# Kernel tuning notes

Hardware: AMD Instinct MI355X
Metric: run time of the kernel (lower is better)

The kernel has to match this reference:

```python
import jax, jax.numpy as jnp
import numpy as np

HQ, HKV, HD = 8, 4, 256          # query heads, kv heads, head dim
SW = 1024                         # sliding window (layer_idx=0 is even -> window active)
EPS = 1e-6
SCALE = 256.0 ** -0.5             # query_pre_attn_scalar ** -0.5
THETA = 10000.0
NEG = jnp.finfo(jnp.float32).min


def _rms_norm(x, w):
    # Gemma2 RMSNorm: fp32 variance, weight applied as (1 + kernel)
    var = jnp.mean(jnp.square(x.astype(jnp.float32)), axis=-1, keepdims=True)
    xn = x / jnp.sqrt(var + EPS)
    return (1.0 + w) * xn


def _rope(q, k, positions):
    # standard rotate-half RoPE over full head_dim
    inv = 1.0 / (THETA ** (jnp.arange(0, HD, 2, dtype=jnp.float32) / HD))  # [HD/2]
    freqs = positions.astype(jnp.float32)[..., None] * inv                  # [B,S,HD/2]
    emb = jnp.concatenate([freqs, freqs], axis=-1)                          # [B,S,HD]
    cos = jnp.cos(emb)[:, :, None, :]
    sin = jnp.sin(emb)[:, :, None, :]
    def rot(x):
        return jnp.concatenate([-x[..., HD // 2:], x[..., :HD // 2]], axis=-1)
    return q * cos + rot(q) * sin, k * cos + rot(k) * sin


def setup_inputs() -> dict:
    key = jax.random.key(0)
    ks = jax.random.split(key, 12)
    B, S, D, I = 1, 2048, 2304, 9216
    std = 0.02
    return {
        "hidden_states": jax.random.normal(ks[0], (B, S, D), jnp.float32),
        "attention_mask": jnp.ones((B, S), jnp.int32),
        "position_ids": jnp.broadcast_to(jnp.arange(S, dtype=jnp.int32)[None], (B, S)),
        "wq": jax.random.normal(ks[1], (D, HQ * HD), jnp.float32) * std,
        "wk": jax.random.normal(ks[2], (D, HKV * HD), jnp.float32) * std,
        "wv": jax.random.normal(ks[3], (D, HKV * HD), jnp.float32) * std,
        "wo": jax.random.normal(ks[4], (HQ * HD, D), jnp.float32) * std,
        "w_gate": jax.random.normal(ks[5], (D, I), jnp.float32) * std,
        "w_up": jax.random.normal(ks[6], (D, I), jnp.float32) * std,
        "w_down": jax.random.normal(ks[7], (I, D), jnp.float32) * std,
        "ln_in": jax.random.uniform(ks[8], (D,), jnp.float32) * 0.1,
        "ln_post_attn": jax.random.uniform(ks[9], (D,), jnp.float32) * 0.1,
        "ln_pre_ffn": jax.random.uniform(ks[10], (D,), jnp.float32) * 0.1,
        "ln_post_ffn": jax.random.uniform(ks[11], (D,), jnp.float32) * 0.1,
    }


def _attention(h, attention_mask, position_ids, wq, wk, wv, wo):
    B, S, _ = h.shape
    q = (h @ wq).reshape(B, S, HQ, HD)
    k = (h @ wk).reshape(B, S, HKV, HD)
    v = (h @ wv).reshape(B, S, HKV, HD)
    q, k = _rope(q, k, position_ids)
    # GQA: repeat kv heads
    groups = HQ // HKV
    k = jnp.repeat(k, groups, axis=2)  # [B,S,HQ,HD]
    v = jnp.repeat(v, groups, axis=2)
    # combined mask: causal AND within sliding window AND padding mask
    i = jnp.arange(S)[:, None]
    j = jnp.arange(S)[None, :]
    keep = (j <= i) & ((i - j) < SW)                       # [S,S]
    keep = keep[None, None] & (attention_mask[:, None, None, :] > 0)  # [B,1,S,S]
    bias = jnp.where(keep, 0.0, NEG).astype(jnp.float32)
    scores = jnp.einsum("bqhd,bkhd->bhqk", q, k) * SCALE + bias
    probs = jax.nn.softmax(scores, axis=-1)
    out = jnp.einsum("bhqk,bkhd->bqhd", probs, v).reshape(B, S, HQ * HD)
    return out @ wo


def reference(hidden_states, attention_mask, position_ids, wq, wk, wv, wo,
              w_gate, w_up, w_down, ln_in, ln_post_attn, ln_pre_ffn, ln_post_ffn):
    # Gemma2 decoder layer with sandwich norms
    residual = hidden_states
    h = _rms_norm(hidden_states, ln_in)
    attn = _attention(h, attention_mask, position_ids, wq, wk, wv, wo)
    h = _rms_norm(attn, ln_post_attn)
    x = residual + h
    residual = x
    h = _rms_norm(x, ln_pre_ffn)
    h = (jax.nn.gelu(h @ w_gate, approximate=True) * (h @ w_up)) @ w_down
    h = _rms_norm(h, ln_post_ffn)
    return residual + h
```

## Files before the change

kernel.cpp:

```cpp
#include <hip/hip_runtime.h>
#include <stdint.h>
#include <type_traits>

typedef unsigned short u16;
typedef unsigned int u32;
typedef __bf16 bf16x8 __attribute__((ext_vector_type(8)));
typedef float f32x4 __attribute__((ext_vector_type(4)));

#define S_LEN 2048
#define DMODEL 2304
#define DFF 9216
#define NHQ 8
#define NHKV 4
#define HDIM 256
#define SWIN 1024

template <int N> using IC = std::integral_constant<int, N>;

__device__ __forceinline__ u16 f2bf(float f) {
  u32 u = __float_as_uint(f);
  u = (u + 0x7FFFu + ((u >> 16) & 1)) >> 16;
  return (u16)u;
}
__device__ __forceinline__ float bf2f(u16 h) {
  return __uint_as_float(((u32)h) << 16);
}

__device__ __forceinline__ void gload_lds16(const void* g, void* l) {
  __builtin_amdgcn_global_load_lds((const __attribute__((address_space(1))) u32*)g,
                                   (__attribute__((address_space(3))) u32*)l, 16, 0, 0);
}

template <int N>
__device__ __forceinline__ void wait_vmcnt() {
  if constexpr (N == 0) asm volatile("s_waitcnt vmcnt(0)" ::: "memory");
  else if constexpr (N == 4) asm volatile("s_waitcnt vmcnt(4)" ::: "memory");
  else if constexpr (N == 5) asm volatile("s_waitcnt vmcnt(5)" ::: "memory");
  else if constexpr (N == 6) asm volatile("s_waitcnt vmcnt(6)" ::: "memory");
  else if constexpr (N == 8) asm volatile("s_waitcnt vmcnt(8)" ::: "memory");
}

__device__ __forceinline__ float gelu_t(float x) {
  float u = 0.7978845608f * (x + 0.044715f * x * x * x);
  float e = __expf(2.f * u);
  float t = 1.f - 2.f / (e + 1.f);
  return 0.5f * x * (1.f + t);
}

__global__ __launch_bounds__(256) void transpose_convert(
    const float* __restrict__ in, u16* __restrict__ out, int K, int N, int stride) {
  __shared__ float t[32][130];
  const int k0 = blockIdx.x * 32, n0 = blockIdx.y * 128;
  const int tx = threadIdx.x & 31, ty = threadIdx.x >> 5;
#pragma unroll
  for (int r = 0; r < 4; ++r) {
    const float4 v = *(const float4*)&in[(size_t)(k0 + ty + r * 8) * stride + n0 + 4 * tx];
    t[ty + r * 8][4 * tx + 0] = v.x;
    t[ty + r * 8][4 * tx + 1] = v.y;
    t[ty + r * 8][4 * tx + 2] = v.z;
    t[ty + r * 8][4 * tx + 3] = v.w;
  }
  __syncthreads();
  const int kk = threadIdx.x & 15, nn = threadIdx.x >> 4;
#pragma unroll
  for (int r = 0; r < 8; ++r) {
    const int n = nn + r * 16;
    const u32 p = (u32)f2bf(t[2 * kk][n]) | ((u32)f2bf(t[2 * kk + 1][n]) << 16);
    *(u32*)&out[(size_t)(n0 + n) * K + k0 + 2 * kk] = p;
  }
}

__global__ __launch_bounds__(256) void vpack_kernel(
    const float* __restrict__ qkvf, u16* __restrict__ vtile) {
  __shared__ float t[32][33];
  const int s0 = blockIdx.x * 32, d0 = blockIdx.y * 32, kvh = blockIdx.z;
  const int tx = threadIdx.x & 31, ty = threadIdx.x >> 5;
#pragma unroll
  for (int r = 0; r < 4; ++r)
    t[ty + r * 8][tx] = qkvf[(size_t)(s0 + ty + r * 8) * 4096 + 3072 + kvh * HDIM + d0 + tx];
  __syncthreads();
  const int kk = threadIdx.x & 15, nn = threadIdx.x >> 4;
#pragma unroll
  for (int r = 0; r < 2; ++r) {
    const int d = nn + r * 16;
    const u32 p = (u32)f2bf(t[2 * kk][d]) | ((u32)f2bf(t[2 * kk + 1][d]) << 16);
    *(u32*)&vtile[(((size_t)kvh * 64 + (s0 >> 5)) * 256 + d0 + d) * 32 + 2 * kk] = p;
  }
}

__device__ __forceinline__ float block_sumsq(const float* xr, int D) {
  float ss = 0.f;
  for (int d = threadIdx.x; d < D; d += 256) { float v = xr[d]; ss += v * v; }
#pragma unroll
  for (int m = 1; m < 64; m <<= 1) ss += __shfl_xor(ss, m, 64);
  __shared__ float red[4];
  if ((threadIdx.x & 63) == 0) red[threadIdx.x >> 6] = ss;
  __syncthreads();
  return red[0] + red[1] + red[2] + red[3];
}

__global__ __launch_bounds__(256) void rmsnorm_bf16_kernel(
    const float* __restrict__ x, const float* __restrict__ w, u16* __restrict__ o) {
  const int row = blockIdx.x;
  const float* xr = x + (size_t)row * DMODEL;
  float tot = block_sumsq(xr, DMODEL);
  float inv = rsqrtf(tot / DMODEL + 1e-6f);
  u16* orow = o + (size_t)row * DMODEL;
  for (int d = threadIdx.x; d < DMODEL; d += 256)
    orow[d] = f2bf((1.f + w[d]) * (xr[d] * inv));
}

__global__ __launch_bounds__(256) void rms_add_rms_kernel(
    const float* __restrict__ y0, const float* __restrict__ y1,
    const float* __restrict__ w1,
    const float* __restrict__ res, const float* __restrict__ w2,
    float* __restrict__ xres, u16* __restrict__ hn) {
  const int row = blockIdx.x;
  const float* yr0 = y0 + (size_t)row * DMODEL;
  const float* yr1 = y1 + (size_t)row * DMODEL;
  const float* rr = res + (size_t)row * DMODEL;
  __shared__ float red[2][4];
  float yv[9];
  float ss = 0.f;
#pragma unroll
  for (int e = 0; e < 9; ++e) {
    const int d = threadIdx.x + e * 256;
    yv[e] = yr0[d] + yr1[d];
    ss += yv[e] * yv[e];
  }
#pragma unroll
  for (int m = 1; m < 64; m <<= 1) ss += __shfl_xor(ss, m, 64);
  if ((threadIdx.x & 63) == 0) red[0][threadIdx.x >> 6] = ss;
  __syncthreads();
  const float inv1 = rsqrtf((red[0][0] + red[0][1] + red[0][2] + red[0][3]) / DMODEL + 1e-6f);
  float* xr = xres + (size_t)row * DMODEL;
  float xv[9];
  float ss2 = 0.f;
#pragma unroll
  for (int e = 0; e < 9; ++e) {
    const int d = threadIdx.x + e * 256;
    float x = rr[d] + (1.f + w1[d]) * (yv[e] * inv1);
    xv[e] = x;
    xr[d] = x;
    ss2 += x * x;
  }
#pragma unroll
  for (int m = 1; m < 64; m <<= 1) ss2 += __shfl_xor(ss2, m, 64);
  if ((threadIdx.x & 63) == 0) red[1][threadIdx.x >> 6] = ss2;
  __syncthreads();
  const float inv2 = rsqrtf((red[1][0] + red[1][1] + red[1][2] + red[1][3]) / DMODEL + 1e-6f);
  u16* hr = hn + (size_t)row * DMODEL;
#pragma unroll
  for (int e = 0; e < 9; ++e) {
    const int d = threadIdx.x + e * 256;
    hr[d] = f2bf((1.f + w2[d]) * (xv[e] * inv2));
  }
}

__global__ __launch_bounds__(256) void reduce8_rms_add_kernel(
    const u16* __restrict__ p, const float* __restrict__ w,
    const float* __restrict__ res, float* __restrict__ o) {
  const int row = blockIdx.x;
  const size_t PS = (size_t)S_LEN * DMODEL;
  const u16* pr = p + (size_t)row * DMODEL;
  float y[9];
  float ss = 0.f;
#pragma unroll
  for (int e = 0; e < 9; ++e) {
    const int d = threadIdx.x + e * 256;
    float v = 0.f;
#pragma unroll
    for (int k = 0; k < 8; ++k) v += bf2f(pr[d + k * PS]);
    y[e] = v;
    ss += v * v;
  }
#pragma unroll
  for (int m = 1; m < 64; m <<= 1) ss += __shfl_xor(ss, m, 64);
  __shared__ float red[4];
  if ((threadIdx.x & 63) == 0) red[threadIdx.x >> 6] = ss;
  __syncthreads();
  const float tot = red[0] + red[1] + red[2] + red[3];
  const float inv = rsqrtf(tot / DMODEL + 1e-6f);
  const float* rr = res + (size_t)row * DMODEL;
  float* orow = o + (size_t)row * DMODEL;
#pragma unroll
  for (int e = 0; e < 9; ++e) {
    const int d = threadIdx.x + e * 256;
    orow[d] = rr[d] + (1.f + w[d]) * (y[e] * inv);
  }
}

__global__ void rope_kernel(const float* __restrict__ qkv, const int* __restrict__ pos,
                            u16* __restrict__ qb, u16* __restrict__ kt) {
  const int s = blockIdx.x;
  const int t = threadIdx.x;
  float p = (float)pos[s];
  float inv = powf(10000.f, -(float)(2 * t) / (float)HDIM);
  float f = p * inv;
  float cs = cosf(f), sn = sinf(f);
  const float* row = qkv + (size_t)s * 4096;
  u16* qr = qb + (size_t)s * (NHQ * HDIM);
#pragma unroll
  for (int h = 0; h < NHQ; ++h) {
    float x1 = row[h * HDIM + t], x2 = row[h * HDIM + t + 128];
    qr[h * HDIM + t] = f2bf(x1 * cs - x2 * sn);
    qr[h * HDIM + t + 128] = f2bf(x2 * cs + x1 * sn);
  }
#pragma unroll
  for (int h = 0; h < NHKV; ++h) {
    u16* kr = kt + ((size_t)h * S_LEN + s) * HDIM;
    float x1 = row[2048 + h * HDIM + t], x2 = row[2048 + h * HDIM + t + 128];
    kr[t] = f2bf(x1 * cs - x2 * sn);
    kr[t + 128] = f2bf(x2 * cs + x1 * sn);
  }
}

template <int BN, int MODE, int BUFS>
__global__ __launch_bounds__(512) void gemm_pipe(
    const u16* __restrict__ A, const u16* __restrict__ Bt, const u16* __restrict__ Bt2,
    void* __restrict__ Cv, void* __restrict__ Cv2,
    int M, int N, int Klen, int LDK, int ntn, int n1,
    const u16* __restrict__ gptr) {
  constexpr bool DUAL = (MODE == 4);
  constexpr int CH_B = BN / 8;
  constexpr int CH_TOT = 16 + (DUAL ? 2 * CH_B : CH_B);
  constexpr int LPW = CH_TOT / 8;
  constexpr int TILE = CH_TOT * 512;
  constexpr int NFR = BN / 64;
  __shared__ __align__(16) u16 smem[BUFS * TILE];

  const int tid = threadIdx.x;
  const int lane = tid & 63, wave = tid >> 6;
  const int wr = wave >> 2, wc = wave & 3;
  const int l15 = lane & 15, l16 = lane >> 4;

  const int MB = M >> 7;
  const int nwg = gridDim.x;
  const int orig = blockIdx.x;
  const int q = nwg >> 3, r = nwg & 7, xcd = orig & 7, lidx = orig >> 3;
  const int wg = (xcd < r ? xcd * (q + 1) : r * (q + 1) + (xcd - r) * q) + lidx;
  const int tiles = MB * ntn;
  const int kz = wg / tiles, wgt = wg % tiles;
  const int bm = wgt % MB, bn = wgt / MB;
  const bool side2 = !DUAL && bn >= n1;
  const int bnl = side2 ? bn - n1 : bn;
  const u16* Bp = side2 ? Bt2 : Bt;

  const u16* Az = A + (size_t)kz * Klen;
  const u16* Bz = Bp + (size_t)kz * Klen;
  const int NT = Klen >> 6;

  const u16* src[LPW];
  const int swz = (((lane & 7) ^ (lane >> 3)) * 8);
#pragma unroll
  for (int i = 0; i < LPW; ++i) {
    const int c = wave * LPW + i;
    if (c < 16) src[i] = Az + (size_t)(bm * 128 + c * 8 + (lane >> 3)) * LDK + swz;
    else if (!DUAL || c < 16 + CH_B)
      src[i] = Bz + (size_t)(bnl * BN + (c - 16) * 8 + (lane >> 3)) * LDK + swz;
    else
      src[i] = Bt2 + (size_t)kz * Klen + (size_t)(bnl * BN + (c - 16 - CH_B) * 8 + (lane >> 3)) * LDK + swz;
  }
  const int dst0 = wave * LPW * 512 + lane * 8;

  auto STAGE = [&](int buf, int kt) {
    u16* base = smem + buf * TILE + dst0;
    const size_t ko = (size_t)kt * 64;
#pragma unroll
    for (int i = 0; i < LPW; ++i) gload_lds16(src[i] + ko, base + i * 512);
  };

  f32x4 acc[4][NFR];
  f32x4 acc2[DUAL ? 4 : 1][DUAL ? NFR : 1];
#pragma unroll
  for (int m = 0; m < 4; ++m)
#pragma unroll
    for (int n = 0; n < NFR; ++n) {
      acc[m][n] = f32x4{0.f, 0.f, 0.f, 0.f};
      if constexpr (DUAL) acc2[m][n] = f32x4{0.f, 0.f, 0.f, 0.f};
    }

  bf16x8 a[2][4], b[2][NFR];
  bf16x8 u[DUAL ? 2 : 1][DUAL ? NFR : 1];

  auto READK = [&](auto kkc, int buf) {
    constexpr int kk = decltype(kkc)::value;
    const u16* Ab = smem + buf * TILE;
    const u16* Bb = Ab + 16 * 512;
    const u16* Ub = Ab + (16 + CH_B) * 512;
    const int cc = kk * 4 + l16;
#pragma unroll
    for (int m = 0; m < 4; ++m) {
      const int rr = wr * 64 + m * 16 + l15;
      a[kk][m] = *(const bf16x8*)&Ab[rr * 64 + ((cc ^ (rr & 7)) * 8)];
    }
#pragma unroll
    for (int n = 0; n < NFR; ++n) {
      const int rr = wc * (BN / 4) + n * 16 + l15;
      b[kk][n] = *(const bf16x8*)&Bb[rr * 64 + ((cc ^ (rr & 7)) * 8)];
      if constexpr (DUAL)
        u[kk][n] = *(const bf16x8*)&Ub[rr * 64 + ((cc ^ (rr & 7)) * 8)];
    }
  };

  auto MFMAK = [&](auto kkc) {
    constexpr int kk = decltype(kkc)::value;
    __builtin_amdgcn_s_setprio(1);
#pragma unroll
    for (int m = 0; m < 4; ++m)
#pragma unroll
      for (int n = 0; n < NFR; ++n)
        acc[m][n] = __builtin_amdgcn_mfma_f32_16x16x32_bf16(a[kk][m], b[kk][n], acc[m][n], 0, 0, 0);
    if constexpr (DUAL) {
#pragma unroll
      for (int m = 0; m < 4; ++m)
#pragma unroll
        for (int n = 0; n < NFR; ++n)
          acc2[m][n] = __builtin_amdgcn_mfma_f32_16x16x32_bf16(a[kk][m], u[kk][n], acc2[m][n], 0, 0, 0);
    }
    __builtin_amdgcn_s_setprio(0);
  };

  if constexpr (BUFS == 2) {
    STAGE(0, 0);
    wait_vmcnt<0>();
    __builtin_amdgcn_s_barrier();
    int cur = 0;
    for (int t = 0; t < NT; ++t) {
      if (t + 1 < NT) STAGE(cur ^ 1, t + 1);
      READK(IC<0>{}, cur);
      READK(IC<1>{}, cur);
      MFMAK(IC<0>{});
      MFMAK(IC<1>{});
      if (t + 1 < NT) { wait_vmcnt<0>(); __builtin_amdgcn_s_barrier(); }
      cur ^= 1;
    }
  } else {
    STAGE(0, 0);
    STAGE(1, 1);
    wait_vmcnt<0>();
    __builtin_amdgcn_s_barrier();
    READK(IC<0>{}, 0);
    int cur = 0;
    for (int t = 0; t < NT; ++t) {
      const int nxt = (cur == 2) ? 0 : cur + 1;
      const int fre = (nxt == 2) ? 0 : nxt + 1;
      if (t + 2 < NT) STAGE(fre, t + 2);
      READK(IC<1>{}, cur);
      MFMAK(IC<0>{});
      if (t + 1 < NT) READK(IC<0>{}, nxt);
      MFMAK(IC<1>{});
      if (t + 1 < NT) { wait_vmcnt<0>(); __builtin_amdgcn_s_barrier(); }
      cur = nxt;
    }
  }

  const int row0 = bm * 128 + wr * 64 + l16 * 4;
  const int col0 = bnl * BN + wc * (BN / 4) + l15;
  float* Cf = (float*)(side2 ? Cv2 : Cv) + (size_t)kz * M * N;
  u16* Cb = (u16*)(side2 ? Cv2 : Cv) + (size_t)kz * M * N;
#pragma unroll
  for (int m = 0; m < 4; ++m)
#pragma unroll
    for (int n = 0; n < NFR; ++n)
#pragma unroll
      for (int rr = 0; rr < 4; ++rr) {
        const size_t idx = (size_t)(row0 + m * 16 + rr) * N + col0 + n * 16;
        if (MODE == 0) Cf[idx] = acc[m][n][rr];
        else if (MODE == 1) Cb[idx] = f2bf(acc[m][n][rr]);
        else if (MODE == 2) ((u16*)Cv)[idx] = f2bf(gelu_t(bf2f(gptr[idx])) * acc[m][n][rr]);
        else if (MODE == 4) {
          if constexpr (DUAL)
            ((u16*)Cv)[idx] = f2bf(gelu_t(acc[m][n][rr]) * acc2[m][n][rr]);
        }
      }
}

__global__ __launch_bounds__(256) void attn_kernel(
    const u16* __restrict__ qb, const u16* __restrict__ kt,
    const u16* __restrict__ vtile, const int* __restrict__ amask,
    u16* __restrict__ outp) {
  __shared__ __align__(16) u16 Ks[2][32 * 256];
  __shared__ __align__(16) u16 Vs[2][256 * 32];
  __shared__ __align__(16) u16 Ps[4][16 * 40];
  const int bid = blockIdx.x;
  const int qh = bid & 7;
  const int qblk = bid >> 3;
  const int kvh = qh >> 1;
  const int q0 = qblk * 64;
  const int tid = threadIdx.x, lane = tid & 63, wave = tid >> 6;
  const int qrow = q0 + wave * 16;
  const int l15 = lane & 15, l16 = lane >> 4;

  bf16x8 qf[8];
  {
    const u16* qp = qb + (size_t)(qrow + l15) * (NHQ * HDIM) + qh * HDIM + l16 * 8;
#pragma unroll
    for (int kc = 0; kc < 8; ++kc) qf[kc] = *(const bf16x8*)(qp + kc * 32);
  }
  f32x4 acc[16];
#pragma unroll
  for (int n = 0; n < 16; ++n) acc[n] = f32x4{0.f, 0.f, 0.f, 0.f};
  float mr[4] = {-1e30f, -1e30f, -1e30f, -1e30f};
  float sr[4] = {0.f, 0.f, 0.f, 0.f};

  int lo = q0 - (SWIN - 1); if (lo < 0) lo = 0; lo &= ~31;
  const int ntiles = ((q0 + 63 - lo) >> 5) + 1;

  const char* kbase = (const char*)(kt + (size_t)kvh * S_LEN * HDIM);
  const char* vbase = (const char*)(vtile + (size_t)kvh * 64 * 256 * 32);

  auto STAGEKV = [&](int buf, int key0) {
    const char* ksrc = kbase + (size_t)key0 * 512;
    const char* vsrc = vbase + (size_t)(key0 >> 5) * 16384;
#pragma unroll
    for (int i = 0; i < 4; ++i) {
      const int b = (wave * 4 + i) * 1024 + lane * 16;
      gload_lds16(ksrc + (b ^ (((b >> 9) & 7) << 4)), (char*)&Ks[buf][0] + (wave * 4 + i) * 1024);
    }
#pragma unroll
    for (int i = 0; i < 4; ++i) {
      const int b = (wave * 4 + i) * 1024 + lane * 16;
      gload_lds16(vsrc + (b ^ (((b >> 6) & 3) << 4)), (char*)&Vs[buf][0] + (wave * 4 + i) * 1024);
    }
  };

  STAGEKV(0, lo);
  wait_vmcnt<0>();
  __builtin_amdgcn_s_barrier();

  int cur = 0;
  for (int it = 0; it < ntiles; ++it) {
    const int key0 = lo + it * 32;
    const int am0 = amask[key0 + l15];
    const int am1 = amask[key0 + 16 + l15];
    if (it + 1 < ntiles) { STAGEKV(cur ^ 1, key0 + 32); wait_vmcnt<8>(); }
    else                 { wait_vmcnt<0>(); }
    __builtin_amdgcn_s_barrier();

    if (key0 <= qrow + 15 && key0 + 31 >= qrow - (SWIN - 1)) {
      f32x4 sc[2];
      sc[0] = f32x4{0.f, 0.f, 0.f, 0.f};
      sc[1] = f32x4{0.f, 0.f, 0.f, 0.f};
#pragma unroll
      for (int ct = 0; ct < 2; ++ct) {
        const int r = ct * 16 + l15;
#pragma unroll
        for (int kc = 0; kc < 8; ++kc) {
          const int byte = (r * 512 + kc * 64 + l16 * 16) ^ ((r & 7) << 4);
          bf16x8 kf = *(const bf16x8*)((const char*)&Ks[cur][0] + byte);
          sc[ct] = __builtin_amdgcn_mfma_f32_16x16x32_bf16(qf[kc], kf, sc[ct], 0, 0, 0);
        }
      }
      float pr[2][4];
#pragma unroll
      for (int ct = 0; ct < 2; ++ct) {
        const int j = key0 + ct * 16 + l15;
        const bool jok = (ct ? am1 : am0) > 0;
#pragma unroll
        for (int r = 0; r < 4; ++r) {
          const int i = qrow + l16 * 4 + r;
          const bool ok = jok && (j <= i) && (i - j < SWIN);
          pr[ct][r] = ok ? sc[ct][r] * 0.0625f : -1e30f;
        }
      }
      float resc[4];
#pragma unroll
      for (int r = 0; r < 4; ++r) {
        float mx = fmaxf(pr[0][r], pr[1][r]);
#pragma unroll
        for (int mm = 1; mm < 16; mm <<= 1) mx = fmaxf(mx, __shfl_xor(mx, mm, 64));
        const float mnew = fmaxf(mr[r], mx);
        const float rs = __expf(mr[r] - mnew);
        mr[r] = mnew;
        float p0 = __expf(pr[0][r] - mnew);
        float p1 = __expf(pr[1][r] - mnew);
        pr[0][r] = p0; pr[1][r] = p1;
        float sm = p0 + p1;
#pragma unroll
        for (int mm = 1; mm < 16; mm <<= 1) sm += __shfl_xor(sm, mm, 64);
        sr[r] = sr[r] * rs + sm;
        resc[r] = rs;
      }
#pragma unroll
      for (int n = 0; n < 16; ++n)
#pragma unroll
        for (int r = 0; r < 4; ++r) acc[n][r] *= resc[r];
      u16* P = &Ps[wave][0];
#pragma unroll
      for (int ct = 0; ct < 2; ++ct)
#pragma unroll
        for (int r = 0; r < 4; ++r)
          P[(l16 * 4 + r) * 40 + ct * 16 + l15] = f2bf(pr[ct][r]);
      bf16x8 pa = *(const bf16x8*)&P[l15 * 40 + l16 * 8];
#pragma unroll
      for (int n = 0; n < 16; ++n) {
        const int d = n * 16 + l15;
        const int byte = (d * 64 + l16 * 16) ^ ((d & 3) << 4);
        bf16x8 vf = *(const bf16x8*)((const char*)&Vs[cur][0] + byte);
        acc[n] = __builtin_amdgcn_mfma_f32_16x16x32_bf16(pa, vf, acc[n], 0, 0, 0);
      }
    }
    __builtin_amdgcn_s_barrier();
    cur ^= 1;
  }
#pragma unroll
  for (int n = 0; n < 16; ++n)
#pragma unroll
    for (int r = 0; r < 4; ++r) {
      const int i = qrow + l16 * 4 + r;
      outp[(size_t)i * (NHQ * HDIM) + qh * HDIM + n * 16 + l15] = f2bf(acc[n][r] / sr[r]);
    }
}

__global__ void gelu_mul_kernel(const u16* __restrict__ g, const u16* __restrict__ u,
                                u16* __restrict__ o, int n8) {
  const int idx0 = blockIdx.x * blockDim.x + threadIdx.x;
  const int stride = gridDim.x * blockDim.x;
  for (int i = idx0; i < n8; i += stride) {
    uint4 gv = ((const uint4*)g)[i];
    uint4 uv = ((const uint4*)u)[i];
    u32 gg[4] = {gv.x, gv.y, gv.z, gv.w};
    u32 uu[4] = {uv.x, uv.y, uv.z, uv.w};
    u32 ow[4];
#pragma unroll
    for (int w = 0; w < 4; ++w) {
      float x0 = bf2f((u16)(gg[w] & 0xffff)), x1 = bf2f((u16)(gg[w] >> 16));
      float y0 = bf2f((u16)(uu[w] & 0xffff)), y1 = bf2f((u16)(uu[w] >> 16));
      ow[w] = (u32)f2bf(gelu_t(x0) * y0) | ((u32)f2bf(gelu_t(x1) * y1) << 16);
    }
    ((uint4*)o)[i] = make_uint4(ow[0], ow[1], ow[2], ow[3]);
  }
}

extern "C" void kernel_launch(void* const* d_in, const int* in_sizes, int n_in,
                              void* d_out, int out_size, void* d_ws, size_t ws_size,
                              hipStream_t stream) {
  const float* hidden = (const float*)d_in[0];
  const int*   amask  = (const int*)d_in[1];
  const int*   pos    = (const int*)d_in[2];
  const float* wq     = (const float*)d_in[3];
  const float* wk     = (const float*)d_in[4];
  const float* wv     = (const float*)d_in[5];
  const float* wo     = (const float*)d_in[6];
  const float* wg     = (const float*)d_in[7];
  const float* wu     = (const float*)d_in[8];
  const float* wd     = (const float*)d_in[9];
  const float* ln_in  = (const float*)d_in[10];
  const float* ln_pa  = (const float*)d_in[11];
  const float* ln_pf  = (const float*)d_in[12];
  const float* ln_po  = (const float*)d_in[13];
  float* out = (float*)d_out;

  char* ws = (char*)d_ws;
  size_t off = 0;
  auto alloc = [&](size_t b) { char* p = ws + off; off += (b + 255) & ~(size_t)255; return p; };
  u16*   WT    = (u16*)alloc((size_t)DFF * DMODEL * 2);
  u16*   hnorm = (u16*)alloc((size_t)S_LEN * DMODEL * 2);
  char*  big0  = alloc((size_t)S_LEN * DFF * 2);
  u16*   qb    = (u16*)alloc((size_t)S_LEN * NHQ * HDIM * 2);
  u16*   ktb   = (u16*)alloc((size_t)NHKV * S_LEN * HDIM * 2);
  u16*   vtile = (u16*)alloc((size_t)NHKV * 64 * 256 * 32 * 2);
  u16*   attn  = (u16*)alloc((size_t)S_LEN * NHQ * HDIM * 2);
  float* f32t  = (float*)alloc((size_t)S_LEN * DMODEL * 4);
  float* xres  = (float*)alloc((size_t)S_LEN * DMODEL * 4);
  u16*   gbuf  = (u16*)alloc((size_t)S_LEN * DFF * 2);
  u16*   ubuf  = (u16*)alloc((size_t)S_LEN * DFF * 2);
  u16*   WTU   = (u16*)alloc((size_t)DFF * DMODEL * 2);
  const bool fused_gu = (off <= ws_size);
  (void)n_in; (void)in_sizes; (void)out_size; (void)f32t;
  float* qkvf = (float*)big0;
  u16*   ggu  = (u16*)big0;
  float* opart = (float*)big0;
  u16*   part = gbuf;
  const size_t PS = (size_t)S_LEN * DMODEL;

  const dim3 B256(256), B128(128), B512(512);

  rmsnorm_bf16_kernel<<<dim3(S_LEN), B256, 0, stream>>>(hidden, ln_in, hnorm);
  transpose_convert<<<dim3(DMODEL / 32, 2048 / 128), B256, 0, stream>>>(wq, WT, DMODEL, 2048, 2048);
  transpose_convert<<<dim3(DMODEL / 32, 1024 / 128), B256, 0, stream>>>(wk, WT + (size_t)2048 * DMODEL, DMODEL, 1024, 1024);
  transpose_convert<<<dim3(DMODEL / 32, 1024 / 128), B256, 0, stream>>>(wv, WT + (size_t)3072 * DMODEL, DMODEL, 1024, 1024);
  gemm_pipe<128, 0, 2><<<dim3(512), B512, 0, stream>>>(hnorm, WT, WT, qkvf, qkvf, S_LEN, 4096, DMODEL, DMODEL, 32, 32, nullptr);
  rope_kernel<<<dim3(S_LEN), B128, 0, stream>>>(qkvf, pos, qb, ktb);
  vpack_kernel<<<dim3(S_LEN / 32, HDIM / 32, NHKV), B256, 0, stream>>>(qkvf, vtile);
  attn_kernel<<<dim3((S_LEN / 64) * NHQ), B256, 0, stream>>>(qb, ktb, vtile, amask, attn);
  transpose_convert<<<dim3(2048 / 32, DMODEL / 128), B256, 0, stream>>>(wo, WT, 2048, DMODEL, DMODEL);
  gemm_pipe<192, 0, 2><<<dim3(384), B512, 0, stream>>>(attn, WT, WT, opart, opart, S_LEN, DMODEL, 1024, 2048, 12, 12, nullptr);
  rms_add_rms_kernel<<<dim3(S_LEN), B256, 0, stream>>>(opart, opart + PS, ln_pa, hidden, ln_pf, xres, hnorm);
  if (fused_gu) {
    transpose_convert<<<dim3(DMODEL / 32, DFF / 128), B256, 0, stream>>>(wg, WT, DMODEL, DFF, DFF);
    transpose_convert<<<dim3(DMODEL / 32, DFF / 128), B256, 0, stream>>>(wu, WTU, DMODEL, DFF, DFF);
    gemm_pipe<128, 4, 3><<<dim3(1152), B512, 0, stream>>>(hnorm, WT, WTU, ggu, nullptr, S_LEN, DFF, DMODEL, DMODEL, 72, 72, nullptr);
  } else {
    transpose_convert<<<dim3(DMODEL / 32, DFF / 128), B256, 0, stream>>>(wg, WT, DMODEL, DFF, DFF);
    gemm_pipe<192, 1, 3><<<dim3(768), B512, 0, stream>>>(hnorm, WT, WT, gbuf, gbuf, S_LEN, DFF, DMODEL, DMODEL, 48, 48, nullptr);
    transpose_convert<<<dim3(DMODEL / 32, DFF / 128), B256, 0, stream>>>(wu, WT, DMODEL, DFF, DFF);
    gemm_pipe<192, 2, 3><<<dim3(768), B512, 0, stream>>>(hnorm, WT, WT, ggu, ggu, S_LEN, DFF, DMODEL, DMODEL, 48, 48, gbuf);
  }
  transpose_convert<<<dim3(DFF / 32, DMODEL / 128), B256, 0, stream>>>(wd, WT, DFF, DMODEL, DMODEL);
  gemm_pipe<192, 1, 2><<<dim3(1536), B512, 0, stream>>>(ggu, WT, WT, part, part, S_LEN, DMODEL, DFF / 8, DFF, 12, 12, nullptr);
  reduce8_rms_add_kernel<<<dim3(S_LEN), B256, 0, stream>>>(part, ln_po, xres, out);
}
```

Before: 643.9 us.

## Load GEMM B operand directly from global into registers, stage only A in LDS

Reworks the pipelined GEMM so that only the A tile is staged through shared memory. Each wave now reads its B (and U, for the dual gate/up GEMM) fragments straight from global memory into registers, which shrinks LDS use and allows higher occupancy via launch-bounds hints. The triple-buffer path is removed, and the fused gate/up GEMM switches from a 128-wide tile on 1152 blocks to a 192-wide tile on 768 blocks. The trade-off is that B loads are no longer shared across waves through LDS and are not coalesced, and the global-load latency is exposed inside the loop with no prefetch.

```diff
diff --git a/kernel.cpp b/kernel.cpp
--- a/kernel.cpp
+++ b/kernel.cpp
@@ -215,19 +215,16 @@
   }
 }
 
-template <int BN, int MODE, int BUFS>
-__global__ __launch_bounds__(512) void gemm_pipe(
+template <int BN, int MODE>
+__global__ __launch_bounds__(512, (MODE == 4) ? 2 : 4) void gemm_pipe(
     const u16* __restrict__ A, const u16* __restrict__ Bt, const u16* __restrict__ Bt2,
     void* __restrict__ Cv, void* __restrict__ Cv2,
     int M, int N, int Klen, int LDK, int ntn, int n1,
     const u16* __restrict__ gptr) {
   constexpr bool DUAL = (MODE == 4);
-  constexpr int CH_B = BN / 8;
-  constexpr int CH_TOT = 16 + (DUAL ? 2 * CH_B : CH_B);
-  constexpr int LPW = CH_TOT / 8;
-  constexpr int TILE = CH_TOT * 512;
+  constexpr int TILE = 16 * 512;
   constexpr int NFR = BN / 64;
-  __shared__ __align__(16) u16 smem[BUFS * TILE];
+  __shared__ __align__(16) u16 smem[2 * TILE];
 
   const int tid = threadIdx.x;
   const int lane = tid & 63, wave = tid >> 6;
@@ -248,27 +245,33 @@
 
   const u16* Az = A + (size_t)kz * Klen;
   const u16* Bz = Bp + (size_t)kz * Klen;
+  const u16* Uz = Bt2 + (size_t)kz * Klen;
   const int NT = Klen >> 6;
 
-  const u16* src[LPW];
+  const u16* src[2];
   const int swz = (((lane & 7) ^ (lane >> 3)) * 8);
 #pragma unroll
-  for (int i = 0; i < LPW; ++i) {
-    const int c = wave * LPW + i;
-    if (c < 16) src[i] = Az + (size_t)(bm * 128 + c * 8 + (lane >> 3)) * LDK + swz;
-    else if (!DUAL || c < 16 + CH_B)
-      src[i] = Bz + (size_t)(bnl * BN + (c - 16) * 8 + (lane >> 3)) * LDK + swz;
-    else
-      src[i] = Bt2 + (size_t)kz * Klen + (size_t)(bnl * BN + (c - 16 - CH_B) * 8 + (lane >> 3)) * LDK + swz;
-  }
-  const int dst0 = wave * LPW * 512 + lane * 8;
+  for (int i = 0; i < 2; ++i) {
+    const int c = wave * 2 + i;
+    src[i] = Az + (size_t)(bm * 128 + c * 8 + (lane >> 3)) * LDK + swz;
+  }
+  const int dst0 = wave * 2 * 512 + lane * 8;
 
   auto STAGE = [&](int buf, int kt) {
     u16* base = smem + buf * TILE + dst0;
     const size_t ko = (size_t)kt * 64;
 #pragma unroll
-    for (int i = 0; i < LPW; ++i) gload_lds16(src[i] + ko, base + i * 512);
+    for (int i = 0; i < 2; ++i) gload_lds16(src[i] + ko, base + i * 512);
   };
+
+  const u16* bp[NFR];
+  const u16* up[DUAL ? NFR : 1];
+#pragma unroll
+  for (int n = 0; n < NFR; ++n) {
+    const int rowb = bnl * BN + wc * (BN / 4) + n * 16 + l15;
+    bp[n] = Bz + (size_t)rowb * LDK + l16 * 8;
+    if constexpr (DUAL) up[n] = Uz + (size_t)rowb * LDK + l16 * 8;
+  }
 
   f32x4 acc[4][NFR];
   f32x4 acc2[DUAL ? 4 : 1][DUAL ? NFR : 1];
@@ -283,24 +286,25 @@
   bf16x8 a[2][4], b[2][NFR];
   bf16x8 u[DUAL ? 2 : 1][DUAL ? NFR : 1];
 
-  auto READK = [&](auto kkc, int buf) {
+  auto LOADB = [&](auto kkc, int kt) {
+    constexpr int kk = decltype(kkc)::value;
+    const size_t ko = (size_t)kt * 64 + kk * 32;
+#pragma unroll
+    for (int n = 0; n < NFR; ++n) {
+      b[kk][n] = *(const bf16x8*)(bp[n] + ko);
+      if constexpr (DUAL) u[kk][n] = *(const bf16x8*)(up[n] + ko);
+    }
+  };
+
+  auto READA = [&](auto kkc, int buf) {
     constexpr int kk = decltype(kkc)::value;
     const u16* Ab = smem + buf * TILE;
-    const u16* Bb = Ab + 16 * 512;
-    const u16* Ub = Ab + (16 + CH_B) * 512;
     const int cc = kk * 4 + l16;
 #pragma unroll
     for (int m = 0; m < 4; ++m) {
       const int rr = wr * 64 + m * 16 + l15;
       a[kk][m] = *(const bf16x8*)&Ab[rr * 64 + ((cc ^ (rr & 7)) * 8)];
     }
-#pragma unroll
-    for (int n = 0; n < NFR; ++n) {
-      const int rr = wc * (BN / 4) + n * 16 + l15;
-      b[kk][n] = *(const bf16x8*)&Bb[rr * 64 + ((cc ^ (rr & 7)) * 8)];
-      if constexpr (DUAL)
-        u[kk][n] = *(const bf16x8*)&Ub[rr * 64 + ((cc ^ (rr & 7)) * 8)];
-    }
   };
 
   auto MFMAK = [&](auto kkc) {
@@ -321,38 +325,20 @@
     __builtin_amdgcn_s_setprio(0);
   };
 
-  if constexpr (BUFS == 2) {
-    STAGE(0, 0);
-    wait_vmcnt<0>();
-    __builtin_amdgcn_s_barrier();
-    int cur = 0;
-    for (int t = 0; t < NT; ++t) {
-      if (t + 1 < NT) STAGE(cur ^ 1, t + 1);
-      READK(IC<0>{}, cur);
-      READK(IC<1>{}, cur);
-      MFMAK(IC<0>{});
-      MFMAK(IC<1>{});
-      if (t + 1 < NT) { wait_vmcnt<0>(); __builtin_amdgcn_s_barrier(); }
-      cur ^= 1;
-    }
-  } else {
-    STAGE(0, 0);
-    STAGE(1, 1);
-    wait_vmcnt<0>();
-    __builtin_amdgcn_s_barrier();
-    READK(IC<0>{}, 0);
-    int cur = 0;
-    for (int t = 0; t < NT; ++t) {
-      const int nxt = (cur == 2) ? 0 : cur + 1;
-      const int fre = (nxt == 2) ? 0 : nxt + 1;
-      if (t + 2 < NT) STAGE(fre, t + 2);
-      READK(IC<1>{}, cur);
-      MFMAK(IC<0>{});
-      if (t + 1 < NT) READK(IC<0>{}, nxt);
-      MFMAK(IC<1>{});
-      if (t + 1 < NT) { wait_vmcnt<0>(); __builtin_amdgcn_s_barrier(); }
-      cur = nxt;
-    }
+  STAGE(0, 0);
+  wait_vmcnt<0>();
+  __builtin_amdgcn_s_barrier();
+  int cur = 0;
+  for (int t = 0; t < NT; ++t) {
+    LOADB(IC<0>{}, t);
+    LOADB(IC<1>{}, t);
+    if (t + 1 < NT) STAGE(cur ^ 1, t + 1);
+    READA(IC<0>{}, cur);
+    READA(IC<1>{}, cur);
+    MFMAK(IC<0>{});
+    MFMAK(IC<1>{});
+    if (t + 1 < NT) { wait_vmcnt<0>(); __builtin_amdgcn_s_barrier(); }
+    cur ^= 1;
   }
 
   const int row0 = bm * 128 + wr * 64 + l16 * 4;
@@ -581,24 +567,24 @@
   transpose_convert<<<dim3(DMODEL / 32, 2048 / 128), B256, 0, stream>>>(wq, WT, DMODEL, 2048, 2048);
   transpose_convert<<<dim3(DMODEL / 32, 1024 / 128), B256, 0, stream>>>(wk, WT + (size_t)2048 * DMODEL, DMODEL, 1024, 1024);
   transpose_convert<<<dim3(DMODEL / 32, 1024 / 128), B256, 0, stream>>>(wv, WT + (size_t)3072 * DMODEL, DMODEL, 1024, 1024);
-  gemm_pipe<128, 0, 2><<<dim3(512), B512, 0, stream>>>(hnorm, WT, WT, qkvf, qkvf, S_LEN, 4096, DMODEL, DMODEL, 32, 32, nullptr);
+  gemm_pipe<128, 0><<<dim3(512), B512, 0, stream>>>(hnorm, WT, WT, qkvf, qkvf, S_LEN, 4096, DMODEL, DMODEL, 32, 32, nullptr);
   rope_kernel<<<dim3(S_LEN), B128, 0, stream>>>(qkvf, pos, qb, ktb);
   vpack_kernel<<<dim3(S_LEN / 32, HDIM / 32, NHKV), B256, 0, stream>>>(qkvf, vtile);
   attn_kernel<<<dim3((S_LEN / 64) * NHQ), B256, 0, stream>>>(qb, ktb, vtile, amask, attn);
   transpose_convert<<<dim3(2048 / 32, DMODEL / 128), B256, 0, stream>>>(wo, WT, 2048, DMODEL, DMODEL);
-  gemm_pipe<192, 0, 2><<<dim3(384), B512, 0, stream>>>(attn, WT, WT, opart, opart, S_LEN, DMODEL, 1024, 2048, 12, 12, nullptr);
+  gemm_pipe<192, 0><<<dim3(384), B512, 0, stream>>>(attn, WT, WT, opart, opart, S_LEN, DMODEL, 1024, 2048, 12, 12, nullptr);
   rms_add_rms_kernel<<<dim3(S_LEN), B256, 0, stream>>>(opart, opart + PS, ln_pa, hidden, ln_pf, xres, hnorm);
   if (fused_gu) {
     transpose_convert<<<dim3(DMODEL / 32, DFF / 128), B256, 0, stream>>>(wg, WT, DMODEL, DFF, DFF);
     transpose_convert<<<dim3(DMODEL / 32, DFF / 128), B256, 0, stream>>>(wu, WTU, DMODEL, DFF, DFF);
-    gemm_pipe<128, 4, 3><<<dim3(1152), B512, 0, stream>>>(hnorm, WT, WTU, ggu, nullptr, S_LEN, DFF, DMODEL, DMODEL, 72, 72, nullptr);
+    gemm_pipe<192, 4><<<dim3(768), B512, 0, stream>>>(hnorm, WT, WTU, ggu, nullptr, S_LEN, DFF, DMODEL, DMODEL, 48, 48, nullptr);
   } else {
     transpose_convert<<<dim3(DMODEL / 32, DFF / 128), B256, 0, stream>>>(wg, WT, DMODEL, DFF, DFF);
-    gemm_pipe<192, 1, 3><<<dim3(768), B512, 0, stream>>>(hnorm, WT, WT, gbuf, gbuf, S_LEN, DFF, DMODEL, DMODEL, 48, 48, nullptr);
+    gemm_pipe<192, 1><<<dim3(768), B512, 0, stream>>>(hnorm, WT, WT, gbuf, gbuf, S_LEN, DFF, DMODEL, DMODEL, 48, 48, nullptr);
     transpose_convert<<<dim3(DMODEL / 32, DFF / 128), B256, 0, stream>>>(wu, WT, DMODEL, DFF, DFF);
-    gemm_pipe<192, 2, 3><<<dim3(768), B512, 0, stream>>>(hnorm, WT, WT, ggu, ggu, S_LEN, DFF, DMODEL, DMODEL, 48, 48, gbuf);
+    gemm_pipe<192, 2><<<dim3(768), B512, 0, stream>>>(hnorm, WT, WT, ggu, ggu, S_LEN, DFF, DMODEL, DMODEL, 48, 48, gbuf);
   }
   transpose_convert<<<dim3(DFF / 32, DMODEL / 128), B256, 0, stream>>>(wd, WT, DFF, DMODEL, DMODEL);
-  gemm_pipe<192, 1, 2><<<dim3(1536), B512, 0, stream>>>(ggu, WT, WT, part, part, S_LEN, DMODEL, DFF / 8, DFF, 12, 12, nullptr);
+  gemm_pipe<192, 1><<<dim3(1536), B512, 0, stream>>>(ggu, WT, WT, part, part, S_LEN, DMODEL, DFF / 8, DFF, 12, 12, nullptr);
   reduce8_rms_add_kernel<<<dim3(S_LEN), B256, 0, stream>>>(part, ln_po, xres, out);
 }
```

New measurement: 959.0 us. +49.0%, slower.

## Restructure two-buffer GEMM pipeline to prefetch two tiles ahead; widen fused gate/up tile

Applied to the files above, without the earlier changes.

The BUFS==2 GEMM path now preloads two k-tiles. Each iteration reads its fragments, then barriers so the current buffer can be refilled with tile t+2. That refill is split into two halves, each interleaved with one MFMA phase, and vmcnt waits allow one tile of loads to stay in flight. The fused gate/up GEMM switches from BN=128 with three buffers to BN=192 with two buffers, giving larger tiles and fewer workgroups. The goal is to hide global-to-LDS latency behind compute. The cost is an extra barrier per iteration and higher register and LDS pressure for the dual-accumulator BN=192 variant, which could reduce occupancy.

```diff
diff --git a/kernel.cpp b/kernel.cpp
--- a/kernel.cpp
+++ b/kernel.cpp
@@ -225,6 +225,7 @@
   constexpr int CH_B = BN / 8;
   constexpr int CH_TOT = 16 + (DUAL ? 2 * CH_B : CH_B);
   constexpr int LPW = CH_TOT / 8;
+  constexpr int H0 = LPW / 2;
   constexpr int TILE = CH_TOT * 512;
   constexpr int NFR = BN / 64;
   __shared__ __align__(16) u16 smem[BUFS * TILE];
@@ -269,6 +270,18 @@
 #pragma unroll
     for (int i = 0; i < LPW; ++i) gload_lds16(src[i] + ko, base + i * 512);
   };
+  auto STAGEH0 = [&](int buf, int kt) {
+    u16* base = smem + buf * TILE + dst0;
+    const size_t ko = (size_t)kt * 64;
+#pragma unroll
+    for (int i = 0; i < H0; ++i) gload_lds16(src[i] + ko, base + i * 512);
+  };
+  auto STAGEH1 = [&](int buf, int kt) {
+    u16* base = smem + buf * TILE + dst0;
+    const size_t ko = (size_t)kt * 64;
+#pragma unroll
+    for (int i = H0; i < LPW; ++i) gload_lds16(src[i] + ko, base + i * 512);
+  };
 
   f32x4 acc[4][NFR];
   f32x4 acc2[DUAL ? 4 : 1][DUAL ? NFR : 1];
@@ -323,16 +336,27 @@
 
   if constexpr (BUFS == 2) {
     STAGE(0, 0);
-    wait_vmcnt<0>();
+    STAGE(1, 1);
+    wait_vmcnt<LPW>();
     __builtin_amdgcn_s_barrier();
     int cur = 0;
     for (int t = 0; t < NT; ++t) {
-      if (t + 1 < NT) STAGE(cur ^ 1, t + 1);
       READK(IC<0>{}, cur);
       READK(IC<1>{}, cur);
+      asm volatile("s_waitcnt lgkmcnt(0)" ::: "memory");
+      __builtin_amdgcn_sched_barrier(0);
+      __builtin_amdgcn_s_barrier();
+      __builtin_amdgcn_sched_barrier(0);
+      const bool pf = (t + 2 < NT);
+      if (pf) STAGEH0(cur, t + 2);
       MFMAK(IC<0>{});
+      if (pf) STAGEH1(cur, t + 2);
       MFMAK(IC<1>{});
-      if (t + 1 < NT) { wait_vmcnt<0>(); __builtin_amdgcn_s_barrier(); }
+      if (t + 1 < NT) {
+        if (pf) wait_vmcnt<LPW>();
+        else    wait_vmcnt<0>();
+        __builtin_amdgcn_s_barrier();
+      }
       cur ^= 1;
     }
   } else {
@@ -591,7 +615,7 @@
   if (fused_gu) {
     transpose_convert<<<dim3(DMODEL / 32, DFF / 128), B256, 0, stream>>>(wg, WT, DMODEL, DFF, DFF);
     transpose_convert<<<dim3(DMODEL / 32, DFF / 128), B256, 0, stream>>>(wu, WTU, DMODEL, DFF, DFF);
-    gemm_pipe<128, 4, 3><<<dim3(1152), B512, 0, stream>>>(hnorm, WT, WTU, ggu, nullptr, S_LEN, DFF, DMODEL, DMODEL, 72, 72, nullptr);
+    gemm_pipe<192, 4, 2><<<dim3(768), B512, 0, stream>>>(hnorm, WT, WTU, ggu, nullptr, S_LEN, DFF, DMODEL, DMODEL, 48, 48, nullptr);
   } else {
     transpose_convert<<<dim3(DMODEL / 32, DFF / 128), B256, 0, stream>>>(wg, WT, DMODEL, DFF, DFF);
     gemm_pipe<192, 1, 3><<<dim3(768), B512, 0, stream>>>(hnorm, WT, WT, gbuf, gbuf, S_LEN, DFF, DMODEL, DMODEL, 48, 48, nullptr);
```

After: 613.7 us. -4.7%, faster.

## Overlap weight transposes with attention and o-proj GEMM via extra blocks

Applied to the files above, without the earlier changes.

Fold the wo, w_gate and w_up fp32-to-bf16 transposes into extra blocks of the attention kernel, and the w_down transpose into extra blocks of the o-projection GEMM. The idea is to fill idle CUs during the small attention and o-proj grids and to drop separate launches. A new direct_transpose does uncoalesced strided loads with no shared memory. The fused gate/up GEMM also switches from BN=128 with 3 buffers to BN=192 with 2 buffers, and intermediate buffers (f32t, gbuf) are reused to hold the transposed weights. The risk is that the heavy transpose blocks interfere with attention and that the strided loads are slow.

```diff
diff --git a/kernel.cpp b/kernel.cpp
--- a/kernel.cpp
+++ b/kernel.cpp
@@ -45,6 +45,32 @@
   float e = __expf(2.f * u);
   float t = 1.f - 2.f / (e + 1.f);
   return 0.5f * x * (1.f + t);
+}
+
+template <int NT>
+__device__ __forceinline__ void direct_transpose(
+    const float* __restrict__ in, u16* __restrict__ out, int K, int N, int t, int nk) {
+  const int k0 = (t % nk) * 32, n0 = (t / nk) * 128;
+  const int tid = (int)threadIdx.x;
+  const int nn = tid >> 2, ch = tid & 3;
+  const int kb = k0 + ch * 8;
+  constexpr int NP = (NT == 256) ? 2 : 1;
+  float x[NP][8];
+#pragma unroll
+  for (int p = 0; p < NP; ++p) {
+    const int n = n0 + nn + p * (NT / 4);
+#pragma unroll
+    for (int j = 0; j < 8; ++j) x[p][j] = in[(size_t)(kb + j) * N + n];
+  }
+#pragma unroll
+  for (int p = 0; p < NP; ++p) {
+    const int n = n0 + nn + p * (NT / 4);
+    u32 w[4];
+#pragma unroll
+    for (int jj = 0; jj < 4; ++jj)
+      w[jj] = (u32)f2bf(x[p][2 * jj]) | ((u32)f2bf(x[p][2 * jj + 1]) << 16);
+    *(uint4*)&out[(size_t)n * K + kb] = make_uint4(w[0], w[1], w[2], w[3]);
+  }
 }
 
 __global__ __launch_bounds__(256) void transpose_convert(
@@ -220,7 +246,13 @@
     const u16* __restrict__ A, const u16* __restrict__ Bt, const u16* __restrict__ Bt2,
     void* __restrict__ Cv, void* __restrict__ Cv2,
     int M, int N, int Klen, int LDK, int ntn, int n1,
-    const u16* __restrict__ gptr) {
+    const u16* __restrict__ gptr,
+    int ggrid, const float* __restrict__ tin, u16* __restrict__ toutT,
+    int tK, int tN, int tnk) {
+  if ((int)blockIdx.x >= ggrid) {
+    direct_transpose<512>(tin, toutT, tK, tN, (int)blockIdx.x - ggrid, tnk);
+    return;
+  }
   constexpr bool DUAL = (MODE == 4);
   constexpr int CH_B = BN / 8;
   constexpr int CH_TOT = 16 + (DUAL ? 2 * CH_B : CH_B);
@@ -235,7 +267,7 @@
   const int l15 = lane & 15, l16 = lane >> 4;
 
   const int MB = M >> 7;
-  const int nwg = gridDim.x;
+  const int nwg = ggrid;
   const int orig = blockIdx.x;
   const int q = nwg >> 3, r = nwg & 7, xcd = orig & 7, lidx = orig >> 3;
   const int wg = (xcd < r ? xcd * (q + 1) : r * (q + 1) + (xcd - r) * q) + lidx;
@@ -379,11 +411,21 @@
 __global__ __launch_bounds__(256) void attn_kernel(
     const u16* __restrict__ qb, const u16* __restrict__ kt,
     const u16* __restrict__ vtile, const int* __restrict__ amask,
-    u16* __restrict__ outp) {
+    u16* __restrict__ outp,
+    const float* __restrict__ t0in, u16* __restrict__ t0out,
+    const float* __restrict__ t1in, u16* __restrict__ t1out,
+    const float* __restrict__ t2in, u16* __restrict__ t2out) {
   __shared__ __align__(16) u16 Ks[2][32 * 256];
   __shared__ __align__(16) u16 Vs[2][256 * 32];
   __shared__ __align__(16) u16 Ps[4][16 * 40];
   const int bid = blockIdx.x;
+  if (bid >= 256) {
+    int t = bid - 256;
+    if (t < 1152)      direct_transpose<256>(t0in, t0out, 2048, 2304, t, 64);
+    else if (t < 6336) direct_transpose<256>(t1in, t1out, 2304, 9216, t - 1152, 72);
+    else               direct_transpose<256>(t2in, t2out, 2304, 9216, t - 6336, 72);
+    return;
+  }
   const int qh = bid & 7;
   const int qblk = bid >> 3;
   const int kvh = qh >> 1;
@@ -568,11 +610,13 @@
   u16*   ubuf  = (u16*)alloc((size_t)S_LEN * DFF * 2);
   u16*   WTU   = (u16*)alloc((size_t)DFF * DMODEL * 2);
   const bool fused_gu = (off <= ws_size);
-  (void)n_in; (void)in_sizes; (void)out_size; (void)f32t;
+  (void)n_in; (void)in_sizes; (void)out_size; (void)ubuf;
   float* qkvf = (float*)big0;
   u16*   ggu  = (u16*)big0;
   float* opart = (float*)big0;
   u16*   part = gbuf;
+  u16*   WTO  = (u16*)f32t;
+  u16*   WTG  = gbuf;
   const size_t PS = (size_t)S_LEN * DMODEL;
 
   const dim3 B256(256), B128(128), B512(512);
@@ -581,24 +625,35 @@
   transpose_convert<<<dim3(DMODEL / 32, 2048 / 128), B256, 0, stream>>>(wq, WT, DMODEL, 2048, 2048);
   transpose_convert<<<dim3(DMODEL / 32, 1024 / 128), B256, 0, stream>>>(wk, WT + (size_t)2048 * DMODEL, DMODEL, 1024, 1024);
   transpose_convert<<<dim3(DMODEL / 32, 1024 / 128), B256, 0, stream>>>(wv, WT + (size_t)3072 * DMODEL, DMODEL, 1024, 1024);
-  gemm_pipe<128, 0, 2><<<dim3(512), B512, 0, stream>>>(hnorm, WT, WT, qkvf, qkvf, S_LEN, 4096, DMODEL, DMODEL, 32, 32, nullptr);
+  gemm_pipe<128, 0, 2><<<dim3(512), B512, 0, stream>>>(hnorm, WT, WT, qkvf, qkvf, S_LEN, 4096, DMODEL, DMODEL, 32, 32, nullptr, 512, nullptr, nullptr, 1, 1, 1);
   rope_kernel<<<dim3(S_LEN), B128, 0, stream>>>(qkvf, pos, qb, ktb);
   vpack_kernel<<<dim3(S_LEN / 32, HDIM / 32, NHKV), B256, 0, stream>>>(qkvf, vtile);
-  attn_kernel<<<dim3((S_LEN / 64) * NHQ), B256, 0, stream>>>(qb, ktb, vtile, amask, attn);
-  transpose_convert<<<dim3(2048 / 32, DMODEL / 128), B256, 0, stream>>>(wo, WT, 2048, DMODEL, DMODEL);
-  gemm_pipe<192, 0, 2><<<dim3(384), B512, 0, stream>>>(attn, WT, WT, opart, opart, S_LEN, DMODEL, 1024, 2048, 12, 12, nullptr);
-  rms_add_rms_kernel<<<dim3(S_LEN), B256, 0, stream>>>(opart, opart + PS, ln_pa, hidden, ln_pf, xres, hnorm);
+
   if (fused_gu) {
+    attn_kernel<<<dim3(256 + 1152 + 5184 + 5184), B256, 0, stream>>>(
+        qb, ktb, vtile, amask, attn, wo, WTO, wg, WTG, wu, WTU);
+    gemm_pipe<192, 0, 2><<<dim3(384 + 5184), B512, 0, stream>>>(
+        attn, WTO, WTO, opart, opart, S_LEN, DMODEL, 1024, 2048, 12, 12, nullptr,
+        384, wd, WT, 9216, 2304, 288);
+    rms_add_rms_kernel<<<dim3(S_LEN), B256, 0, stream>>>(opart, opart + PS, ln_pa, hidden, ln_pf, xres, hnorm);
+    gemm_pipe<192, 4, 2><<<dim3(768), B512, 0, stream>>>(
+        hnorm, WTG, WTU, ggu, nullptr, S_LEN, DFF, DMODEL, DMODEL, 48, 48, nullptr,
+        768, nullptr, nullptr, 1, 1, 1);
+    gemm_pipe<192, 1, 2><<<dim3(1536), B512, 0, stream>>>(
+        ggu, WT, WT, part, part, S_LEN, DMODEL, DFF / 8, DFF, 12, 12, nullptr,
+        1536, nullptr, nullptr, 1, 1, 1);
+  } else {
+    attn_kernel<<<dim3(256), B256, 0, stream>>>(qb, ktb, vtile, amask, attn,
+                                                nullptr, nullptr, nullptr, nullptr, nullptr, nullptr);
+    transpose_convert<<<dim3(2048 / 32, DMODEL / 128), B256, 0, stream>>>(wo, WT, 2048, DMODEL, DMODEL);
+    gemm_pipe<192, 0, 2><<<dim3(384), B512, 0, stream>>>(attn, WT, WT, opart, opart, S_LEN, DMODEL, 1024, 2048, 12, 12, nullptr, 384, nullptr, nullptr, 1, 1, 1);
+    rms_add_rms_kernel<<<dim3(S_LEN), B256, 0, stream>>>(opart, opart + PS, ln_pa, hidden, ln_pf, xres, hnorm);
     transpose_convert<<<dim3(DMODEL / 32, DFF / 128), B256, 0, stream>>>(wg, WT, DMODEL, DFF, DFF);
-    transpose_convert<<<dim3(DMODEL / 32, DFF / 128), B256, 0, stream>>>(wu, WTU, DMODEL, DFF, DFF);
-    gemm_pipe<128, 4, 3><<<dim3(1152), B512, 0, stream>>>(hnorm, WT, WTU, ggu, nullptr, S_LEN, DFF, DMODEL, DMODEL, 72, 72, nullptr);
-  } else {
-    transpose_convert<<<dim3(DMODEL / 32, DFF / 128), B256, 0, stream>>>(wg, WT, DMODEL, DFF, DFF);
-    gemm_pipe<192, 1, 3><<<dim3(768), B512, 0, stream>>>(hnorm, WT, WT, gbuf, gbuf, S_LEN, DFF, DMODEL, DMODEL, 48, 48, nullptr);
+    gemm_pipe<192, 1, 3><<<dim3(768), B512, 0, stream>>>(hnorm, WT, WT, gbuf, gbuf, S_LEN, DFF, DMODEL, DMODEL, 48, 48, nullptr, 768, nullptr, nullptr, 1, 1, 1);
     transpose_convert<<<dim3(DMODEL / 32, DFF / 128), B256, 0, stream>>>(wu, WT, DMODEL, DFF, DFF);
-    gemm_pipe<192, 2, 3><<<dim3(768), B512, 0, stream>>>(hnorm, WT, WT, ggu, ggu, S_LEN, DFF, DMODEL, DMODEL, 48, 48, gbuf);
-  }
-  transpose_convert<<<dim3(DFF / 32, DMODEL / 128), B256, 0, stream>>>(wd, WT, DFF, DMODEL, DMODEL);
-  gemm_pipe<192, 1, 2><<<dim3(1536), B512, 0, stream>>>(ggu, WT, WT, part, part, S_LEN, DMODEL, DFF / 8, DFF, 12, 12, nullptr);
+    gemm_pipe<192, 2, 3><<<dim3(768), B512, 0, stream>>>(hnorm, WT, WT, ggu, ggu, S_LEN, DFF, DMODEL, DMODEL, 48, 48, gbuf, 768, nullptr, nullptr, 1, 1, 1);
+    transpose_convert<<<dim3(DFF / 32, DMODEL / 128), B256, 0, stream>>>(wd, WT, DFF, DMODEL, DMODEL);
+    gemm_pipe<192, 1, 2><<<dim3(1536), B512, 0, stream>>>(ggu, WT, WT, part, part, S_LEN, DMODEL, DFF / 8, DFF, 12, 12, nullptr, 1536, nullptr, nullptr, 1, 1, 1);
+  }
   reduce8_rms_add_kernel<<<dim3(S_LEN), B256, 0, stream>>>(part, ln_po, xres, out);
 }
```

New measurement: 659.9 us. 1.02x slower.
